# Performance work log

Measured on AMD Instinct MI355X. Metric: run time of the kernel, lower is better.

The kernel has to match this reference:

```python
import jax, jax.numpy as jnp
import numpy as np

B, T, L, E, H, V = 128, 16, 196, 512, 1024, 32000


def setup_inputs() -> dict:
    key = jax.random.key(0)
    ks = jax.random.split(key, 20)
    s = 0.02
    return {
        "caption_in": jax.random.randint(ks[0], (B, T), 0, V),
        "image_feats": jax.random.normal(ks[1], (B, L, E), jnp.float32),
        "emb": jax.random.normal(ks[2], (V, E), jnp.float32) * s,
        "W_init_h": jax.random.normal(ks[3], (E, H), jnp.float32) * s,
        "b_init_h": jnp.zeros((H,), jnp.float32),
        "W_init_c": jax.random.normal(ks[4], (E, H), jnp.float32) * s,
        "b_init_c": jnp.zeros((H,), jnp.float32),
        "W_a": jax.random.normal(ks[5], (H, H), jnp.float32) * s,
        "b_a": jnp.zeros((H,), jnp.float32),
        "U_a": jax.random.normal(ks[6], (E, H), jnp.float32) * s,
        "b_ua": jnp.zeros((H,), jnp.float32),
        "V_a": jax.random.normal(ks[7], (H, 1), jnp.float32) * s,
        "b_va": jnp.zeros((1,), jnp.float32),
        "W_beta": jax.random.normal(ks[8], (H, E), jnp.float32) * s,
        "b_beta": jnp.zeros((E,), jnp.float32),
        "W_lstm": jax.random.normal(ks[9], (2 * E, 4 * H), jnp.float32) * s,
        "U_lstm": jax.random.normal(ks[10], (H, 4 * H), jnp.float32) * s,
        "b_lstm": jnp.zeros((4 * H,), jnp.float32),
        "W_out": jax.random.normal(ks[11], (H, V), jnp.float32) * s,
        "b_out": jnp.zeros((V,), jnp.float32),
    }


def _decode(caption_in, image_feats, emb, W_init_h, b_init_h, W_init_c, b_init_c,
            W_a, b_a, U_a, b_ua, V_a, b_va, W_beta, b_beta,
            W_lstm, U_lstm, b_lstm, W_out, b_out):
    cap_emb = emb[caption_in]                      # [B,T,E]
    mean_a = jnp.mean(image_feats, axis=1)         # [B,E]
    h0 = mean_a @ W_init_h + b_init_h              # [B,H]
    c0 = mean_a @ W_init_c + b_init_c
    # attention keys: precompute U_a(h_list) once (same math as in-loop)
    keys = jnp.einsum('ble,eh->blh', image_feats, U_a) + b_ua  # [B,L,H]

    def step(carry, x_t):                          # x_t: [B,E]
        h, c = carry
        q = h @ W_a + b_a                          # [B,H]
        e = jax.nn.relu(q[:, None, :] + keys) @ V_a + b_va  # [B,L,1]
        alpha = jax.nn.softmax(e, axis=1)          # [B,L,1]
        z = jnp.sum(alpha * image_feats, axis=1)   # [B,E]
        z = z * jax.nn.sigmoid(h @ W_beta + b_beta)
        ctx = jnp.concatenate([z, x_t], axis=-1)   # [B,2E]
        gates = ctx @ W_lstm + h @ U_lstm + b_lstm # [B,4H]
        i, f, g, o = jnp.split(gates, 4, axis=-1)  # keras order i,f,c,o
        c_new = jax.nn.sigmoid(f) * c + jax.nn.sigmoid(i) * jnp.tanh(g)
        h_new = jax.nn.sigmoid(o) * jnp.tanh(c_new)
        out = jax.nn.softmax(h_new @ W_out + b_out, axis=-1)  # [B,V]
        return (h_new, c_new), out

    xs = jnp.transpose(cap_emb, (1, 0, 2))         # [T,B,E]
    _, outs = jax.lax.scan(step, (h0, c0), xs)     # [T,B,V]
    return jnp.transpose(outs, (1, 0, 2))          # [B,T,V]


def reference(caption_in, image_feats, emb, W_init_h, b_init_h, W_init_c, b_init_c,
              W_a, b_a, U_a, b_ua, V_a, b_va, W_beta, b_beta,
              W_lstm, U_lstm, b_lstm, W_out, b_out):
    return _decode(caption_in, image_feats, emb, W_init_h, b_init_h, W_init_c, b_init_c,
                   W_a, b_a, U_a, b_ua, V_a, b_va, W_beta, b_beta,
                   W_lstm, U_lstm, b_lstm, W_out, b_out)
```

## Files before the change

### kernel.cpp

```cpp
#include <hip/hip_runtime.h>
#include <hip/hip_bf16.h>
#include <math.h>

constexpr int Bc = 128, Tc = 16, Lc = 196, Ec = 512, Hc = 1024, Vc = 32000;

typedef float f32x4_t __attribute__((ext_vector_type(4)));
typedef short s16x8_t __attribute__((ext_vector_type(8)));

__device__ __forceinline__ float sigmoidf_(float x) { return 1.0f / (1.0f + expf(-x)); }

__device__ __forceinline__ unsigned short bf16rn(float x) {
    union { float f; unsigned u; } v; v.f = x;
    unsigned r = v.u + 0x7fffu + ((v.u >> 16) & 1u);
    return (unsigned short)(r >> 16);
}
__device__ __forceinline__ float bf16tof(unsigned short h) {
    union { unsigned u; float f; } v; v.u = ((unsigned)h) << 16; return v.f;
}

struct TDesc {
    const float* src;
    unsigned short* dhi;
    unsigned short* dlo;
    int N, ldd, gx, base;
};
struct PrepP {
    TDesc d[8];
    int tblocks;
    const float* feats;
    float* mean_a;
};

__global__ __launch_bounds__(256)
void prep_multi(PrepP p)
{
    const int id = blockIdx.x;
    if (id >= p.tblocks) {
        int idm = id - p.tblocks;
        int b = idm >> 1;
        int e = (idm & 1) * 256 + threadIdx.x;
        const float* f = p.feats + ((size_t)b * Lc) * Ec + e;
        float s = 0.f;
        for (int l = 0; l < Lc; ++l) s += f[(size_t)l * Ec];
        p.mean_a[b * Ec + e] = s * (1.0f / Lc);
        return;
    }
    int di = 0;
#pragma unroll
    for (int i = 1; i < 8; ++i) if (id >= p.d[i].base) di = i;
    const TDesc d = p.d[di];
    const int lid = id - d.base;
    const int k0 = (lid % d.gx) * 32;
    const int n0 = (lid / d.gx) * 32;

    __shared__ float tile[32][33];
    const int tx = threadIdx.x & 31, ty = threadIdx.x >> 5;
#pragma unroll
    for (int i = 0; i < 4; ++i)
        tile[ty + i * 8][tx] = d.src[(size_t)(k0 + ty + i * 8) * d.N + n0 + tx];
    __syncthreads();
#pragma unroll
    for (int i = 0; i < 4; ++i) {
        int nl = ty + i * 8;
        float v = tile[tx][nl];
        unsigned short hi = bf16rn(v);
        unsigned short lo = bf16rn(v - bf16tof(hi));
        size_t off = (size_t)(n0 + nl) * d.ldd + k0 + tx;
        d.dhi[off] = hi;
        d.dlo[off] = lo;
    }
}

struct GemmP {
    const float* A;
    const unsigned short* Bhi;
    const unsigned short* Blo;
    float* C;
    const float* bias;
    long ldc, cslice;
    int lda, K, gx, gy, S;
};

__device__ __forceinline__ void gemm_body(char* smem, int bx, int by, int ksl, const GemmP& p)
{
    auto As_hi = (unsigned short (*)[128][32])(smem);
    auto As_lo = (unsigned short (*)[128][32])(smem + 16384);
    auto Bs_hi = (unsigned short (*)[128][32])(smem + 32768);
    auto Bs_lo = (unsigned short (*)[128][32])(smem + 49152);

    const int t = threadIdx.x;
    const int wave = t >> 6, lane = t & 63;
    const int wr = wave >> 1, wc = wave & 1;
    const int lm = lane & 15, qd = lane >> 4;
    const size_t m0 = (size_t)bx * 128;
    const size_t n0 = (size_t)by * 128;

    const int Ksl = p.K / p.S;
    const int kbase = ksl * Ksl;

    const int srow = t >> 1;
    const int skh  = (t & 1) * 16;

    const float* Ap = p.A + (m0 + srow) * (size_t)p.lda + skh + kbase;
    const unsigned short* Bhp = p.Bhi + (n0 + srow) * (size_t)p.K + skh + kbase;
    const unsigned short* Blp = p.Blo + (n0 + srow) * (size_t)p.K + skh + kbase;

    const int nk = Ksl >> 5;
    float* Cp = p.C + (size_t)ksl * p.cslice;

    f32x4_t acc[4][4];
#pragma unroll
    for (int i = 0; i < 4; ++i)
#pragma unroll
        for (int j = 0; j < 4; ++j)
            acc[i][j] = (f32x4_t){0.f, 0.f, 0.f, 0.f};

    float av[16];
    s16x8_t sbh0, sbh1, sbl0, sbl1;

#define G_LOAD(k0_)                                              \
    do {                                                         \
        *(float4*)&av[0]  = *(const float4*)(Ap + (k0_));        \
        *(float4*)&av[4]  = *(const float4*)(Ap + (k0_) + 4);    \
        *(float4*)&av[8]  = *(const float4*)(Ap + (k0_) + 8);    \
        *(float4*)&av[12] = *(const float4*)(Ap + (k0_) + 12);   \
        sbh0 = *(const s16x8_t*)(Bhp + (k0_));                   \
        sbh1 = *(const s16x8_t*)(Bhp + (k0_) + 8);               \
        sbl0 = *(const s16x8_t*)(Blp + (k0_));                   \
        sbl1 = *(const s16x8_t*)(Blp + (k0_) + 8);               \
    } while (0)

#define LDS_STORE(buf_)                                          \
    do {                                                         \
        s16x8_t h0, h1, l0, l1;                                  \
        _Pragma("unroll")                                        \
        for (int i = 0; i < 8; ++i) {                            \
            unsigned short hi = bf16rn(av[i]);                   \
            h0[i] = (short)hi;                                   \
            l0[i] = (short)bf16rn(av[i] - bf16tof(hi));          \
        }                                                        \
        _Pragma("unroll")                                        \
        for (int i = 0; i < 8; ++i) {                            \
            unsigned short hi = bf16rn(av[8 + i]);               \
            h1[i] = (short)hi;                                   \
            l1[i] = (short)bf16rn(av[8 + i] - bf16tof(hi));      \
        }                                                        \
        *(s16x8_t*)&As_hi[buf_][srow][skh]     = h0;             \
        *(s16x8_t*)&As_hi[buf_][srow][skh + 8] = h1;             \
        *(s16x8_t*)&As_lo[buf_][srow][skh]     = l0;             \
        *(s16x8_t*)&As_lo[buf_][srow][skh + 8] = l1;             \
        *(s16x8_t*)&Bs_hi[buf_][srow][skh]     = sbh0;           \
        *(s16x8_t*)&Bs_hi[buf_][srow][skh + 8] = sbh1;           \
        *(s16x8_t*)&Bs_lo[buf_][srow][skh]     = sbl0;           \
        *(s16x8_t*)&Bs_lo[buf_][srow][skh + 8] = sbl1;           \
    } while (0)

    G_LOAD(0);
    LDS_STORE(0);
    if (nk > 1) G_LOAD(32);
    __syncthreads();

    for (int k = 0; k < nk; ++k) {
        const int cur = k & 1;
        s16x8_t ah[4], al[4], bh[4], bl[4];
#pragma unroll
        for (int mt = 0; mt < 4; ++mt) {
            ah[mt] = *(const s16x8_t*)&As_hi[cur][wr * 64 + mt * 16 + lm][qd * 8];
            al[mt] = *(const s16x8_t*)&As_lo[cur][wr * 64 + mt * 16 + lm][qd * 8];
        }
#pragma unroll
        for (int nt = 0; nt < 4; ++nt) {
            bh[nt] = *(const s16x8_t*)&Bs_hi[cur][wc * 64 + nt * 16 + lm][qd * 8];
            bl[nt] = *(const s16x8_t*)&Bs_lo[cur][wc * 64 + nt * 16 + lm][qd * 8];
        }
        if (k + 1 < nk) {
            LDS_STORE(cur ^ 1);
            if (k + 2 < nk) G_LOAD((k + 2) << 5);
        }
#pragma unroll
        for (int mt = 0; mt < 4; ++mt)
#pragma unroll
            for (int nt = 0; nt < 4; ++nt) {
                acc[mt][nt] = __builtin_amdgcn_mfma_f32_16x16x32_bf16(ah[mt], bh[nt], acc[mt][nt], 0, 0, 0);
                acc[mt][nt] = __builtin_amdgcn_mfma_f32_16x16x32_bf16(ah[mt], bl[nt], acc[mt][nt], 0, 0, 0);
                acc[mt][nt] = __builtin_amdgcn_mfma_f32_16x16x32_bf16(al[mt], bh[nt], acc[mt][nt], 0, 0, 0);
            }
        __syncthreads();
    }
#undef G_LOAD
#undef LDS_STORE

#pragma unroll
    for (int nt = 0; nt < 4; ++nt) {
        size_t n = n0 + wc * 64 + nt * 16 + lm;
        float bs = p.bias ? p.bias[n] : 0.f;
#pragma unroll
        for (int mt = 0; mt < 4; ++mt) {
#pragma unroll
            for (int r = 0; r < 4; ++r) {
                size_t m = m0 + wr * 64 + mt * 16 + qd * 4 + r;
                Cp[(size_t)m * p.ldc + n] = acc[mt][nt][r] + bs;
            }
        }
    }
}

__global__ __launch_bounds__(256)
void gemm_one(GemmP p)
{
    __shared__ __align__(16) char smem[65536];
    gemm_body(smem, blockIdx.x, blockIdx.y, blockIdx.z, p);
}

__global__ __launch_bounds__(256)
void gemm_dual(GemmP a, GemmP b)
{
    __shared__ __align__(16) char smem[65536];
    int id = blockIdx.x;
    const int na = a.gx * a.gy * a.S;
    if (id < na) {
        int by = id % a.gy; int bx = (id / a.gy) % a.gx; int kz = id / (a.gy * a.gx);
        gemm_body(smem, bx, by, kz, a);
    } else {
        id -= na;
        int by = id % b.gy; int bx = (id / b.gy) % b.gx; int kz = id / (b.gy * b.gx);
        gemm_body(smem, bx, by, kz, b);
    }
}

__global__ __launch_bounds__(256)
void concat2(const float* __restrict__ a, int na, const float* __restrict__ b, int nb,
             float* __restrict__ out)
{
    int i = blockIdx.x * 256 + threadIdx.x;
    if (i < na) out[i] = a[i];
    else if (i < na + nb) out[i] = b[i - na];
}

__global__ __launch_bounds__(256)
void mean_kernel(const float* __restrict__ feats, float* __restrict__ mean_a)
{
    int b = blockIdx.x;
    int e = blockIdx.y * 256 + threadIdx.x;
    const float* f = feats + ((size_t)b * Lc) * Ec + e;
    float s = 0.f;
    for (int l = 0; l < Lc; ++l) s += f[(size_t)l * Ec];
    mean_a[b * Ec + e] = s * (1.0f / Lc);
}

__global__ __launch_bounds__(256)
void att_scores_sk(const float* __restrict__ qp, long qstride,
                   const float* __restrict__ b_a,
                   const float* __restrict__ keys,
                   const float* __restrict__ V_a, const float* __restrict__ b_va,
                   float* __restrict__ e)
{
    int pair = blockIdx.x * 4 + (threadIdx.x >> 6);
    int lane = threadIdx.x & 63;
    int b = pair / Lc;
    const float* kp = keys + (size_t)pair * Hc;
    const float* q0 = qp + (size_t)b * 1536;
    float s = 0.f;
    for (int h = lane; h < Hc; h += 64) {
        float q = b_a[h] + q0[h] + q0[qstride + h] + q0[2 * qstride + h] + q0[3 * qstride + h];
        s = fmaf(fmaxf(q + kp[h], 0.f), V_a[h], s);
    }
#pragma unroll
    for (int off = 32; off > 0; off >>= 1) s += __shfl_down(s, off);
    if (lane == 0) e[pair] = s + b_va[0];
}

__global__ __launch_bounds__(1024)
void smv_att(float* __restrict__ out, int t,
             const float* __restrict__ qp, long qstride,
             const float* __restrict__ b_a,
             const float* __restrict__ keys,
             const float* __restrict__ V_a, const float* __restrict__ b_va,
             float* __restrict__ e)
{
    __shared__ float red[1024];
    if (blockIdx.x < 128) {
        int b = blockIdx.x;
        float* p = out + ((size_t)b * Tc + t) * (size_t)Vc;
        int tid = threadIdx.x;
        float m = -1e30f;
        for (int v = tid; v < Vc; v += 1024) m = fmaxf(m, p[v]);
        red[tid] = m; __syncthreads();
        for (int s = 512; s > 0; s >>= 1) { if (tid < s) red[tid] = fmaxf(red[tid], red[tid + s]); __syncthreads(); }
        m = red[0]; __syncthreads();
        float sum = 0.f;
        for (int v = tid; v < Vc; v += 1024) sum += expf(p[v] - m);
        red[tid] = sum; __syncthreads();
        for (int s = 512; s > 0; s >>= 1) { if (tid < s) red[tid] += red[tid + s]; __syncthreads(); }
        float inv = 1.0f / red[0];
        for (int v = tid; v < Vc; v += 1024) p[v] = expf(p[v] - m) * inv;
    } else {
        int wave = threadIdx.x >> 6, lane = threadIdx.x & 63;
        int pair = (blockIdx.x - 128) * 16 + wave;
        int b = pair / Lc;
        const float* kp = keys + (size_t)pair * Hc;
        const float* q0 = qp + (size_t)b * 1536;
        float s = 0.f;
        for (int h = lane; h < Hc; h += 64) {
            float q = b_a[h] + q0[h] + q0[qstride + h] + q0[2 * qstride + h] + q0[3 * qstride + h];
            s = fmaf(fmaxf(q + kp[h], 0.f), V_a[h], s);
        }
#pragma unroll
        for (int off = 32; off > 0; off >>= 1) s += __shfl_down(s, off);
        if (lane == 0) e[pair] = s + b_va[0];
    }
}

__global__ __launch_bounds__(256)
void zxcat_fused(const float* __restrict__ e,
                 const float* __restrict__ qp, long qstride,
                 const float* __restrict__ b_beta,
                 const int* __restrict__ caption, const float* __restrict__ emb,
                 const float* __restrict__ feats, const float* __restrict__ hc,
                 float* __restrict__ xcat, int t)
{
    int b = blockIdx.x;
    int j = blockIdx.y * 256 + threadIdx.x;
    if (blockIdx.y < 2) {
        __shared__ float red[256];
        __shared__ float alpha[Lc];
        int tid = threadIdx.x;
        float ev = (tid < Lc) ? e[b * Lc + tid] : -1e30f;
        red[tid] = ev; __syncthreads();
        for (int s = 128; s > 0; s >>= 1) { if (tid < s) red[tid] = fmaxf(red[tid], red[tid + s]); __syncthreads(); }
        float m = red[0]; __syncthreads();
        float ex = (tid < Lc) ? expf(ev - m) : 0.f;
        red[tid] = ex; __syncthreads();
        for (int s = 128; s > 0; s >>= 1) { if (tid < s) red[tid] += red[tid + s]; __syncthreads(); }
        float ssum = red[0];
        if (tid < Lc) alpha[tid] = ex / ssum;
        __syncthreads();
        const float* f = feats + ((size_t)b * Lc) * Ec + j;
        float s = 0.f;
        for (int l = 0; l < Lc; ++l) s = fmaf(alpha[l], f[(size_t)l * Ec], s);
        const float* q0 = qp + (size_t)b * 1536 + 1024 + j;
        float sb = b_beta[j] + q0[0] + q0[qstride] + q0[2 * qstride] + q0[3 * qstride];
        xcat[(size_t)b * 2048 + j] = s * sigmoidf_(sb);
    } else if (j < 2 * Ec) {
        int tok = caption[b * Tc + t];
        xcat[(size_t)b * 2048 + j] = emb[(size_t)tok * Ec + (j - Ec)];
    } else {
        xcat[(size_t)b * 2048 + j] = hc[(size_t)b * 2048 + (j - 2 * Ec)];
    }
}

__global__ __launch_bounds__(256)
void lstm_elem_sk(const float* __restrict__ gp, long gstride,
                  const float* __restrict__ b_lstm,
                  float* __restrict__ hbase, float* __restrict__ cbase, int ld)
{
    int idx = blockIdx.x * 256 + threadIdx.x;
    int b = idx >> 10;
    int j = idx & (Hc - 1);
    float gi = b_lstm[j], gf = b_lstm[Hc + j], gg = b_lstm[2 * Hc + j], go = b_lstm[3 * Hc + j];
#pragma unroll
    for (int s = 0; s < 4; ++s) {
        const float* g = gp + (size_t)s * gstride + (size_t)b * 4 * Hc;
        gi += g[j]; gf += g[Hc + j]; gg += g[2 * Hc + j]; go += g[3 * Hc + j];
    }
    float* cp = cbase + (size_t)b * ld + j;
    float* hp = hbase + (size_t)b * ld + j;
    float cn = sigmoidf_(gf) * (*cp) + sigmoidf_(gi) * tanhf(gg);
    *cp = cn;
    *hp = sigmoidf_(go) * tanhf(cn);
}

__global__ __launch_bounds__(1024)
void softmax_V(float* __restrict__ out, int t)
{
    int b = blockIdx.x;
    float* p = out + ((size_t)b * Tc + t) * (size_t)Vc;
    __shared__ float red[1024];
    int tid = threadIdx.x;
    float m = -1e30f;
    for (int v = tid; v < Vc; v += 1024) m = fmaxf(m, p[v]);
    red[tid] = m; __syncthreads();
    for (int s = 512; s > 0; s >>= 1) { if (tid < s) red[tid] = fmaxf(red[tid], red[tid + s]); __syncthreads(); }
    m = red[0]; __syncthreads();
    float sum = 0.f;
    for (int v = tid; v < Vc; v += 1024) sum += expf(p[v] - m);
    red[tid] = sum; __syncthreads();
    for (int s = 512; s > 0; s >>= 1) { if (tid < s) red[tid] += red[tid + s]; __syncthreads(); }
    float inv = 1.0f / red[0];
    for (int v = tid; v < Vc; v += 1024) p[v] = expf(p[v] - m) * inv;
}

__global__ __launch_bounds__(256)
void att_scores(const float* __restrict__ q, int ldq, const float* __restrict__ keys,
                const float* __restrict__ V_a, const float* __restrict__ b_va,
                float* __restrict__ e)
{
    int pair = blockIdx.x * 4 + (threadIdx.x >> 6);
    int lane = threadIdx.x & 63;
    int b = pair / Lc;
    const float* qp = q + (size_t)b * ldq;
    const float* kp = keys + (size_t)pair * Hc;
    float s = 0.f;
    for (int h = lane; h < Hc; h += 64)
        s = fmaf(fmaxf(qp[h] + kp[h], 0.f), V_a[h], s);
#pragma unroll
    for (int off = 32; off > 0; off >>= 1) s += __shfl_down(s, off);
    if (lane == 0) e[pair] = s + b_va[0];
}

__global__ __launch_bounds__(256)
void softmax_L(float* __restrict__ e)
{
    int b = blockIdx.x;
    float* p = e + b * Lc;
    __shared__ float red[256];
    int tid = threadIdx.x;
    float m = -1e30f;
    if (tid < Lc) m = p[tid];
    red[tid] = m; __syncthreads();
    for (int s = 128; s > 0; s >>= 1) { if (tid < s) red[tid] = fmaxf(red[tid], red[tid + s]); __syncthreads(); }
    m = red[0]; __syncthreads();
    float ex = 0.f;
    if (tid < Lc) ex = expf(p[tid] - m);
    red[tid] = ex; __syncthreads();
    for (int s = 128; s > 0; s >>= 1) { if (tid < s) red[tid] += red[tid + s]; __syncthreads(); }
    if (tid < Lc) p[tid] = ex / red[0];
}

__global__ __launch_bounds__(256)
void z_kernel(const float* __restrict__ alpha, const float* __restrict__ feats,
              float* __restrict__ z)
{
    int b = blockIdx.x;
    int e = blockIdx.y * 256 + threadIdx.x;
    const float* f = feats + ((size_t)b * Lc) * Ec + e;
    const float* a = alpha + b * Lc;
    float s = 0.f;
    for (int l = 0; l < Lc; ++l) s = fmaf(a[l], f[(size_t)l * Ec], s);
    z[b * Ec + e] = s;
}

__global__ __launch_bounds__(256)
void ctx_build(const float* __restrict__ z, const float* __restrict__ sb,
               const int* __restrict__ caption, const float* __restrict__ emb,
               float* __restrict__ ctx, int t)
{
    int b = blockIdx.x;
    int j = blockIdx.y * 256 + threadIdx.x;
    float v;
    if (j < Ec) {
        v = z[b * Ec + j] * sigmoidf_(sb[b * Ec + j]);
    } else {
        int tok = caption[b * Tc + t];
        v = emb[(size_t)tok * Ec + (j - Ec)];
    }
    ctx[b * (2 * Ec) + j] = v;
}

__global__ __launch_bounds__(256)
void lstm_elem(const float* __restrict__ gates, float* __restrict__ hbase,
               float* __restrict__ cbase, int ld)
{
    int idx = blockIdx.x * 256 + threadIdx.x;
    int b = idx >> 10;
    int j = idx & (Hc - 1);
    const float* g = gates + (size_t)b * 4 * Hc;
    float gi = g[j], gf = g[Hc + j], gg = g[2 * Hc + j], go = g[3 * Hc + j];
    float* cp = cbase + (size_t)b * ld + j;
    float* hp = hbase + (size_t)b * ld + j;
    float cn = sigmoidf_(gf) * (*cp) + sigmoidf_(gi) * tanhf(gg);
    *cp = cn;
    *hp = sigmoidf_(go) * tanhf(cn);
}

__global__ __launch_bounds__(256)
void gemm_f32(const float* __restrict__ A, int lda,
              const float* __restrict__ Bm, int ldb,
              float* __restrict__ C, int ldc,
              const float* __restrict__ bias,
              int K, int accumulate)
{
    __shared__ __align__(16) float As[16][68];
    __shared__ __align__(16) float Bs[16][68];
    const int t  = threadIdx.x;
    const int tx = t & 15;
    const int ty = t >> 4;
    const size_t m0 = (size_t)blockIdx.x * 64;
    const size_t n0 = (size_t)blockIdx.y * 64;
    const int arow = t >> 2;
    const int acol = (t & 3) << 2;
    const int brow = t >> 4;
    const int bcol = (t & 15) << 2;
    const float* Aptr = A + (m0 + arow) * (size_t)lda + acol;
    const float* Bptr = Bm + (size_t)brow * ldb + n0 + bcol;
    float acc[4][4] = {};
    for (int k0 = 0; k0 < K; k0 += 16) {
        float4 av = *reinterpret_cast<const float4*>(Aptr + k0);
        float4 bv = *reinterpret_cast<const float4*>(Bptr + (size_t)k0 * ldb);
        As[acol + 0][arow] = av.x;
        As[acol + 1][arow] = av.y;
        As[acol + 2][arow] = av.z;
        As[acol + 3][arow] = av.w;
        *reinterpret_cast<float4*>(&Bs[brow][bcol]) = bv;
        __syncthreads();
#pragma unroll
        for (int k = 0; k < 16; ++k) {
            float4 a4 = *reinterpret_cast<const float4*>(&As[k][ty << 2]);
            float4 b4 = *reinterpret_cast<const float4*>(&Bs[k][tx << 2]);
            float aa[4] = {a4.x, a4.y, a4.z, a4.w};
            float bb[4] = {b4.x, b4.y, b4.z, b4.w};
#pragma unroll
            for (int i = 0; i < 4; ++i)
#pragma unroll
                for (int j = 0; j < 4; ++j)
                    acc[i][j] = fmaf(aa[i], bb[j], acc[i][j]);
        }
        __syncthreads();
    }
    float4 bv4 = {0.f, 0.f, 0.f, 0.f};
    if (bias) bv4 = *reinterpret_cast<const float4*>(&bias[n0 + (tx << 2)]);
#pragma unroll
    for (int i = 0; i < 4; ++i) {
        size_t off = (m0 + (size_t)(ty << 2) + i) * (size_t)ldc + n0 + (tx << 2);
        float4 o;
        o.x = acc[i][0] + bv4.x;
        o.y = acc[i][1] + bv4.y;
        o.z = acc[i][2] + bv4.z;
        o.w = acc[i][3] + bv4.w;
        if (accumulate) {
            float4 prev = *reinterpret_cast<const float4*>(&C[off]);
            o.x += prev.x; o.y += prev.y; o.z += prev.z; o.w += prev.w;
        }
        *reinterpret_cast<float4*>(&C[off]) = o;
    }
}

extern "C" void kernel_launch(void* const* d_in, const int* in_sizes, int n_in,
                              void* d_out, int out_size, void* d_ws, size_t ws_size,
                              hipStream_t stream)
{
    const int*   caption  = (const int*)  d_in[0];
    const float* feats    = (const float*)d_in[1];
    const float* emb      = (const float*)d_in[2];
    const float* W_init_h = (const float*)d_in[3];
    const float* b_init_h = (const float*)d_in[4];
    const float* W_init_c = (const float*)d_in[5];
    const float* b_init_c = (const float*)d_in[6];
    const float* W_a      = (const float*)d_in[7];
    const float* b_a      = (const float*)d_in[8];
    const float* U_a      = (const float*)d_in[9];
    const float* b_ua     = (const float*)d_in[10];
    const float* V_a      = (const float*)d_in[11];
    const float* b_va     = (const float*)d_in[12];
    const float* W_beta   = (const float*)d_in[13];
    const float* b_beta   = (const float*)d_in[14];
    const float* W_lstm   = (const float*)d_in[15];
    const float* U_lstm   = (const float*)d_in[16];
    const float* b_lstm   = (const float*)d_in[17];
    const float* W_out    = (const float*)d_in[18];
    const float* b_out    = (const float*)d_in[19];
    float* out = (float*)d_out;

    dim3 blk(256);

    char* base = (char*)d_ws;
    size_t off = 0;
    auto alloc = [&](size_t bytes) { char* p = base + off; off = (off + bytes + 15) & ~(size_t)15; return p; };

    float* keys      = (float*)alloc((size_t)Bc * Lc * Hc * 4);
    float* hc        = (float*)alloc((size_t)Bc * 2048 * 4);
    float* qsb_part  = (float*)alloc((size_t)4 * Bc * 1536 * 4);
    float* e         = (float*)alloc((size_t)Bc * Lc * 4);
    float* xcat      = (float*)alloc((size_t)Bc * 2048 * 4);
    float* gate_part = (float*)alloc((size_t)4 * Bc * 4 * Hc * 4);
    float* mean_a    = (float*)alloc((size_t)Bc * Ec * 4);
    float* bcat_i    = (float*)alloc(2048 * 4);
    unsigned short* Wout_hi  = (unsigned short*)alloc((size_t)Vc * Hc * 2);
    unsigned short* Wout_lo  = (unsigned short*)alloc((size_t)Vc * Hc * 2);
    unsigned short* Wg_hi    = (unsigned short*)alloc((size_t)4096 * 2048 * 2);
    unsigned short* Wg_lo    = (unsigned short*)alloc((size_t)4096 * 2048 * 2);
    unsigned short* Wqsb_hi  = (unsigned short*)alloc((size_t)1536 * 1024 * 2);
    unsigned short* Wqsb_lo  = (unsigned short*)alloc((size_t)1536 * 1024 * 2);
    unsigned short* Ua_hi    = (unsigned short*)alloc((size_t)1024 * 512 * 2);
    unsigned short* Ua_lo    = (unsigned short*)alloc((size_t)1024 * 512 * 2);
    unsigned short* Wini_hi  = (unsigned short*)alloc((size_t)2048 * 512 * 2);
    unsigned short* Wini_lo  = (unsigned short*)alloc((size_t)2048 * 512 * 2);
    const size_t need_fast = off;

    const long QSTRIDE = (long)Bc * 1536;
    const long GSTRIDE = (long)Bc * 4 * Hc;

    if (ws_size >= need_fast) {
        PrepP pp;
        int pb = 0;
        auto addT = [&](const float* src, int N, unsigned short* dhi, unsigned short* dlo,
                        int ldd, int gx, int gy, int slot) {
            pp.d[slot] = TDesc{src, dhi, dlo, N, ldd, gx, pb};
            pb += gx * gy;
        };
        addT(W_out,    Vc,   Wout_hi, Wout_lo, 1024, 32, 1000, 0);
        addT(W_lstm,   4096, Wg_hi,   Wg_lo,   2048, 32, 128, 1);
        addT(U_lstm,   4096, Wg_hi + 1024, Wg_lo + 1024, 2048, 32, 128, 2);
        addT(W_a,      1024, Wqsb_hi, Wqsb_lo, 1024, 32, 32, 3);
        addT(W_beta,   512,  Wqsb_hi + (size_t)1024 * 1024, Wqsb_lo + (size_t)1024 * 1024, 1024, 32, 16, 4);
        addT(U_a,      1024, Ua_hi,   Ua_lo,   512, 16, 32, 5);
        addT(W_init_h, 1024, Wini_hi, Wini_lo, 512, 16, 32, 6);
        addT(W_init_c, 1024, Wini_hi + (size_t)1024 * 512, Wini_lo + (size_t)1024 * 512, 512, 16, 32, 7);
        pp.tblocks = pb;
        pp.feats = feats;
        pp.mean_a = mean_a;
        prep_multi<<<dim3(pb + 256), blk, 0, stream>>>(pp);
        concat2<<<dim3(8), blk, 0, stream>>>(b_init_h, 1024, b_init_c, 1024, bcat_i);

        auto mkg = [](const float* A, int lda, const unsigned short* bh, const unsigned short* bl,
                      float* C, long ldc, const float* bias, int K, long cslice,
                      int gx, int gy, int S) {
            GemmP p; p.A = A; p.lda = lda; p.Bhi = bh; p.Blo = bl; p.C = C; p.ldc = ldc;
            p.bias = bias; p.K = K; p.cslice = cslice; p.gx = gx; p.gy = gy; p.S = S; return p;
        };
        GemmP g_init = mkg(mean_a, Ec, Wini_hi, Wini_lo, hc, 2048, bcat_i, 512, 0, 1, 16, 1);
        GemmP g_keys = mkg(feats, Ec, Ua_hi, Ua_lo, keys, Hc, b_ua, 512, 0, 196, 8, 1);
        GemmP g_qsb  = mkg(hc, 2048, Wqsb_hi, Wqsb_lo, qsb_part, 1536, nullptr, 1024, QSTRIDE, 1, 12, 4);
        GemmP g_gate = mkg(xcat, 2048, Wg_hi, Wg_lo, gate_part, 4096, nullptr, 2048, GSTRIDE, 1, 32, 4);

        gemm_one<<<dim3(1, 16, 1), blk, 0, stream>>>(g_init);
        gemm_dual<<<dim3(196 * 8 + 48), blk, 0, stream>>>(g_keys, g_qsb);
        att_scores_sk<<<dim3((Bc * Lc) / 4), blk, 0, stream>>>(qsb_part, QSTRIDE, b_a, keys, V_a, b_va, e);

        for (int t = 0; t < Tc; ++t) {
            zxcat_fused<<<dim3(Bc, 8), blk, 0, stream>>>(e, qsb_part, QSTRIDE, b_beta, caption, emb, feats, hc, xcat, t);
            gemm_one<<<dim3(1, 32, 4), blk, 0, stream>>>(g_gate);
            lstm_elem_sk<<<dim3((Bc * Hc) / 256), blk, 0, stream>>>(gate_part, GSTRIDE, b_lstm, hc, hc + 1024, 2048);
            GemmP g_wout = mkg(hc, 2048, Wout_hi, Wout_lo, out + (size_t)t * Vc, (long)Tc * Vc, b_out, 1024, 0, 1, 250, 1);
            if (t < Tc - 1)
                gemm_dual<<<dim3(250 + 48), blk, 0, stream>>>(g_wout, g_qsb);
            else
                gemm_one<<<dim3(1, 250, 1), blk, 0, stream>>>(g_wout);
            int natt = (t < Tc - 1) ? (Bc * Lc) / 16 : 0;
            smv_att<<<dim3(128 + natt), dim3(1024), 0, stream>>>(out, t, qsb_part, QSTRIDE, b_a, keys, V_a, b_va, e);
        }
        return;
    }

    float* ws = (float*)d_ws;
    size_t foff = 0;
    float* l_keys  = ws + foff; foff += (size_t)Bc * Lc * Hc;
    float* l_h     = ws + foff; foff += (size_t)Bc * Hc;
    float* l_c     = ws + foff; foff += (size_t)Bc * Hc;
    float* l_q     = ws + foff; foff += (size_t)Bc * Hc;
    float* l_e     = ws + foff; foff += (size_t)Bc * Lc;
    float* l_sb    = ws + foff; foff += (size_t)Bc * Ec;
    float* l_z     = ws + foff; foff += (size_t)Bc * Ec;
    float* l_ctx   = ws + foff; foff += (size_t)Bc * 2 * Ec;
    float* l_gates = ws + foff; foff += (size_t)Bc * 4 * Hc;
    float* l_mean  = ws + foff; foff += (size_t)Bc * Ec;
    if (ws_size < foff * sizeof(float)) return;

    mean_kernel<<<dim3(Bc, 2), blk, 0, stream>>>(feats, l_mean);
    gemm_f32<<<dim3(Bc / 64, Hc / 64), blk, 0, stream>>>(l_mean, Ec, W_init_h, Hc, l_h, Hc, b_init_h, Ec, 0);
    gemm_f32<<<dim3(Bc / 64, Hc / 64), blk, 0, stream>>>(l_mean, Ec, W_init_c, Hc, l_c, Hc, b_init_c, Ec, 0);
    gemm_f32<<<dim3((Bc * Lc) / 64, Hc / 64), blk, 0, stream>>>(feats, Ec, U_a, Hc, l_keys, Hc, b_ua, Ec, 0);
    for (int t = 0; t < Tc; ++t) {
        gemm_f32<<<dim3(Bc / 64, Hc / 64), blk, 0, stream>>>(l_h, Hc, W_a, Hc, l_q, Hc, b_a, Hc, 0);
        att_scores<<<dim3((Bc * Lc) / 4), blk, 0, stream>>>(l_q, Hc, l_keys, V_a, b_va, l_e);
        softmax_L<<<dim3(Bc), blk, 0, stream>>>(l_e);
        z_kernel<<<dim3(Bc, 2), blk, 0, stream>>>(l_e, feats, l_z);
        gemm_f32<<<dim3(Bc / 64, Ec / 64), blk, 0, stream>>>(l_h, Hc, W_beta, Ec, l_sb, Ec, b_beta, Hc, 0);
        ctx_build<<<dim3(Bc, 4), blk, 0, stream>>>(l_z, l_sb, caption, emb, l_ctx, t);
        gemm_f32<<<dim3(Bc / 64, (4 * Hc) / 64), blk, 0, stream>>>(l_ctx, 2 * Ec, W_lstm, 4 * Hc, l_gates, 4 * Hc, b_lstm, 2 * Ec, 0);
        gemm_f32<<<dim3(Bc / 64, (4 * Hc) / 64), blk, 0, stream>>>(l_h, Hc, U_lstm, 4 * Hc, l_gates, 4 * Hc, nullptr, Hc, 1);
        lstm_elem<<<dim3((Bc * Hc) / 256), blk, 0, stream>>>(l_gates, l_h, l_c, Hc);
        gemm_f32<<<dim3(Bc / 64, Vc / 64), blk, 0, stream>>>(l_h, Hc, W_out, Vc, out + (size_t)t * Vc, Tc * Vc, b_out, Hc, 0);
        softmax_V<<<dim3(Bc), dim3(1024), 0, stream>>>(out, t);
    }
}
```

Baseline: 2.972 ms.

## Fuse attention scores, softmax and context into one per-batch kernel; precompute embeddings

Attention scoring, its softmax and the weighted context sum now run in one 1024-thread block per batch row, fused with the vocab softmax launch. This drops the separate zxcat_fused launch per step. Caption embeddings for all steps are gathered once up front into a per-step xcat buffer, and the LSTM kernel writes h directly into the next step's xcat slice. The intent is to cut one launch per step plus the global round-trip of e, at the cost of fewer, heavier attention blocks (128 instead of 1568) and a larger xcat allocation.

```diff
diff --git a/kernel.cpp b/kernel.cpp
--- a/kernel.cpp
+++ b/kernel.cpp
@@ -249,40 +249,39 @@
 }
 
 __global__ __launch_bounds__(256)
-void att_scores_sk(const float* __restrict__ qp, long qstride,
-                   const float* __restrict__ b_a,
-                   const float* __restrict__ keys,
-                   const float* __restrict__ V_a, const float* __restrict__ b_va,
-                   float* __restrict__ e)
-{
-    int pair = blockIdx.x * 4 + (threadIdx.x >> 6);
-    int lane = threadIdx.x & 63;
-    int b = pair / Lc;
-    const float* kp = keys + (size_t)pair * Hc;
-    const float* q0 = qp + (size_t)b * 1536;
-    float s = 0.f;
-    for (int h = lane; h < Hc; h += 64) {
-        float q = b_a[h] + q0[h] + q0[qstride + h] + q0[2 * qstride + h] + q0[3 * qstride + h];
-        s = fmaf(fmaxf(q + kp[h], 0.f), V_a[h], s);
-    }
-#pragma unroll
-    for (int off = 32; off > 0; off >>= 1) s += __shfl_down(s, off);
-    if (lane == 0) e[pair] = s + b_va[0];
+void xemb_h0(const int* __restrict__ caption, const float* __restrict__ emb,
+             const float* __restrict__ hc, float* __restrict__ xcat)
+{
+    const int nemb = Tc * Bc * 2;
+    int id = blockIdx.x;
+    if (id < nemb) {
+        int t = id >> 8;
+        int r = id & 255;
+        int b = r >> 1;
+        int j = (r & 1) * 256 + threadIdx.x;
+        int tok = caption[b * Tc + t];
+        xcat[(size_t)t * Bc * 2048 + (size_t)b * 2048 + 512 + j] = emb[(size_t)tok * Ec + j];
+    } else {
+        int idx = (id - nemb) * 256 + threadIdx.x;
+        int b = idx >> 10;
+        int j = idx & 1023;
+        xcat[(size_t)b * 2048 + 1024 + j] = hc[(size_t)b * 2048 + j];
+    }
 }
 
 __global__ __launch_bounds__(1024)
-void smv_att(float* __restrict__ out, int t,
-             const float* __restrict__ qp, long qstride,
-             const float* __restrict__ b_a,
-             const float* __restrict__ keys,
-             const float* __restrict__ V_a, const float* __restrict__ b_va,
-             float* __restrict__ e)
+void smv_attz(float* __restrict__ out, int t, int nsmv,
+              const float* __restrict__ qp, long qstride,
+              const float* __restrict__ b_a, const float* __restrict__ b_beta,
+              const float* __restrict__ keys,
+              const float* __restrict__ V_a, const float* __restrict__ b_va,
+              const float* __restrict__ feats, float* __restrict__ xcat_t)
 {
     __shared__ float red[1024];
-    if (blockIdx.x < 128) {
+    const int tid = threadIdx.x;
+    if (blockIdx.x < (unsigned)nsmv) {
         int b = blockIdx.x;
         float* p = out + ((size_t)b * Tc + t) * (size_t)Vc;
-        int tid = threadIdx.x;
         float m = -1e30f;
         for (int v = tid; v < Vc; v += 1024) m = fmaxf(m, p[v]);
         red[tid] = m; __syncthreads();
@@ -294,65 +293,58 @@
         for (int s = 512; s > 0; s >>= 1) { if (tid < s) red[tid] += red[tid + s]; __syncthreads(); }
         float inv = 1.0f / red[0];
         for (int v = tid; v < Vc; v += 1024) p[v] = expf(p[v] - m) * inv;
-    } else {
-        int wave = threadIdx.x >> 6, lane = threadIdx.x & 63;
-        int pair = (blockIdx.x - 128) * 16 + wave;
-        int b = pair / Lc;
-        const float* kp = keys + (size_t)pair * Hc;
-        const float* q0 = qp + (size_t)b * 1536;
-        float s = 0.f;
-        for (int h = lane; h < Hc; h += 64) {
-            float q = b_a[h] + q0[h] + q0[qstride + h] + q0[2 * qstride + h] + q0[3 * qstride + h];
-            s = fmaf(fmaxf(q + kp[h], 0.f), V_a[h], s);
-        }
-#pragma unroll
-        for (int off = 32; off > 0; off >>= 1) s += __shfl_down(s, off);
-        if (lane == 0) e[pair] = s + b_va[0];
-    }
-}
-
-__global__ __launch_bounds__(256)
-void zxcat_fused(const float* __restrict__ e,
-                 const float* __restrict__ qp, long qstride,
-                 const float* __restrict__ b_beta,
-                 const int* __restrict__ caption, const float* __restrict__ emb,
-                 const float* __restrict__ feats, const float* __restrict__ hc,
-                 float* __restrict__ xcat, int t)
-{
-    int b = blockIdx.x;
-    int j = blockIdx.y * 256 + threadIdx.x;
-    if (blockIdx.y < 2) {
-        __shared__ float red[256];
-        __shared__ float alpha[Lc];
-        int tid = threadIdx.x;
-        float ev = (tid < Lc) ? e[b * Lc + tid] : -1e30f;
-        red[tid] = ev; __syncthreads();
-        for (int s = 128; s > 0; s >>= 1) { if (tid < s) red[tid] = fmaxf(red[tid], red[tid + s]); __syncthreads(); }
-        float m = red[0]; __syncthreads();
-        float ex = (tid < Lc) ? expf(ev - m) : 0.f;
-        red[tid] = ex; __syncthreads();
-        for (int s = 128; s > 0; s >>= 1) { if (tid < s) red[tid] += red[tid + s]; __syncthreads(); }
-        float ssum = red[0];
-        if (tid < Lc) alpha[tid] = ex / ssum;
-        __syncthreads();
-        const float* f = feats + ((size_t)b * Lc) * Ec + j;
+        return;
+    }
+    __shared__ float q_lds[Hc];
+    __shared__ float va_lds[Hc];
+    __shared__ float sb_lds[Ec];
+    __shared__ float e_sm[256];
+    __shared__ float alpha[Lc];
+    const int b = blockIdx.x - nsmv;
+    const float* q0 = qp + (size_t)b * 1536;
+    q_lds[tid] = b_a[tid] + q0[tid] + q0[qstride + tid] + q0[2 * qstride + tid] + q0[3 * qstride + tid];
+    va_lds[tid] = V_a[tid];
+    if (tid < Ec) {
+        const float* qs = q0 + 1024 + tid;
+        sb_lds[tid] = b_beta[tid] + qs[0] + qs[qstride] + qs[2 * qstride] + qs[3 * qstride];
+    }
+    __syncthreads();
+    {
+        int wave = tid >> 6, lane = tid & 63;
+        float bva = b_va[0];
+        for (int l = wave; l < Lc; l += 16) {
+            const float* kp = keys + ((size_t)b * Lc + l) * Hc;
+            float s = 0.f;
+            for (int h = lane; h < Hc; h += 64)
+                s = fmaf(fmaxf(q_lds[h] + kp[h], 0.f), va_lds[h], s);
+#pragma unroll
+            for (int off = 32; off > 0; off >>= 1) s += __shfl_down(s, off);
+            if (lane == 0) e_sm[l] = s + bva;
+        }
+    }
+    __syncthreads();
+    float ev = (tid < Lc) ? e_sm[tid] : -1e30f;
+    red[tid] = ev; __syncthreads();
+    for (int s = 512; s > 0; s >>= 1) { if (tid < s) red[tid] = fmaxf(red[tid], red[tid + s]); __syncthreads(); }
+    float m = red[0]; __syncthreads();
+    float ex = (tid < Lc) ? expf(ev - m) : 0.f;
+    red[tid] = ex; __syncthreads();
+    for (int s = 512; s > 0; s >>= 1) { if (tid < s) red[tid] += red[tid + s]; __syncthreads(); }
+    if (tid < Lc) alpha[tid] = ex / red[0];
+    __syncthreads();
+    if (tid < Ec) {
+        const float* f = feats + ((size_t)b * Lc) * Ec + tid;
         float s = 0.f;
         for (int l = 0; l < Lc; ++l) s = fmaf(alpha[l], f[(size_t)l * Ec], s);
-        const float* q0 = qp + (size_t)b * 1536 + 1024 + j;
-        float sb = b_beta[j] + q0[0] + q0[qstride] + q0[2 * qstride] + q0[3 * qstride];
-        xcat[(size_t)b * 2048 + j] = s * sigmoidf_(sb);
-    } else if (j < 2 * Ec) {
-        int tok = caption[b * Tc + t];
-        xcat[(size_t)b * 2048 + j] = emb[(size_t)tok * Ec + (j - Ec)];
-    } else {
-        xcat[(size_t)b * 2048 + j] = hc[(size_t)b * 2048 + (j - 2 * Ec)];
+        xcat_t[(size_t)b * 2048 + tid] = s * sigmoidf_(sb_lds[tid]);
     }
 }
 
 __global__ __launch_bounds__(256)
 void lstm_elem_sk(const float* __restrict__ gp, long gstride,
                   const float* __restrict__ b_lstm,
-                  float* __restrict__ hbase, float* __restrict__ cbase, int ld)
+                  float* __restrict__ hbase, float* __restrict__ cbase, int ld,
+                  float* __restrict__ xh)
 {
     int idx = blockIdx.x * 256 + threadIdx.x;
     int b = idx >> 10;
@@ -364,10 +356,11 @@
         gi += g[j]; gf += g[Hc + j]; gg += g[2 * Hc + j]; go += g[3 * Hc + j];
     }
     float* cp = cbase + (size_t)b * ld + j;
-    float* hp = hbase + (size_t)b * ld + j;
     float cn = sigmoidf_(gf) * (*cp) + sigmoidf_(gi) * tanhf(gg);
     *cp = cn;
-    *hp = sigmoidf_(go) * tanhf(cn);
+    float hn = sigmoidf_(go) * tanhf(cn);
+    hbase[(size_t)b * ld + j] = hn;
+    if (xh) xh[(size_t)b * 2048 + 1024 + j] = hn;
 }
 
 __global__ __launch_bounds__(1024)
@@ -570,8 +563,7 @@
     float* keys      = (float*)alloc((size_t)Bc * Lc * Hc * 4);
     float* hc        = (float*)alloc((size_t)Bc * 2048 * 4);
     float* qsb_part  = (float*)alloc((size_t)4 * Bc * 1536 * 4);
-    float* e         = (float*)alloc((size_t)Bc * Lc * 4);
-    float* xcat      = (float*)alloc((size_t)Bc * 2048 * 4);
+    float* xcat      = (float*)alloc((size_t)Tc * Bc * 2048 * 4);
     float* gate_part = (float*)alloc((size_t)4 * Bc * 4 * Hc * 4);
     float* mean_a    = (float*)alloc((size_t)Bc * Ec * 4);
     float* bcat_i    = (float*)alloc(2048 * 4);
@@ -589,6 +581,7 @@
 
     const long QSTRIDE = (long)Bc * 1536;
     const long GSTRIDE = (long)Bc * 4 * Hc;
+    const size_t XSLICE = (size_t)Bc * 2048;
 
     if (ws_size >= need_fast) {
         PrepP pp;
@@ -621,23 +614,27 @@
         GemmP g_init = mkg(mean_a, Ec, Wini_hi, Wini_lo, hc, 2048, bcat_i, 512, 0, 1, 16, 1);
         GemmP g_keys = mkg(feats, Ec, Ua_hi, Ua_lo, keys, Hc, b_ua, 512, 0, 196, 8, 1);
         GemmP g_qsb  = mkg(hc, 2048, Wqsb_hi, Wqsb_lo, qsb_part, 1536, nullptr, 1024, QSTRIDE, 1, 12, 4);
-        GemmP g_gate = mkg(xcat, 2048, Wg_hi, Wg_lo, gate_part, 4096, nullptr, 2048, GSTRIDE, 1, 32, 4);
 
         gemm_one<<<dim3(1, 16, 1), blk, 0, stream>>>(g_init);
+        xemb_h0<<<dim3(Tc * Bc * 2 + Bc * 4), blk, 0, stream>>>(caption, emb, hc, xcat);
         gemm_dual<<<dim3(196 * 8 + 48), blk, 0, stream>>>(g_keys, g_qsb);
-        att_scores_sk<<<dim3((Bc * Lc) / 4), blk, 0, stream>>>(qsb_part, QSTRIDE, b_a, keys, V_a, b_va, e);
+        smv_attz<<<dim3(Bc), dim3(1024), 0, stream>>>(out, 0, 0, qsb_part, QSTRIDE, b_a, b_beta,
+                                                      keys, V_a, b_va, feats, xcat);
 
         for (int t = 0; t < Tc; ++t) {
-            zxcat_fused<<<dim3(Bc, 8), blk, 0, stream>>>(e, qsb_part, QSTRIDE, b_beta, caption, emb, feats, hc, xcat, t);
+            GemmP g_gate = mkg(xcat + (size_t)t * XSLICE, 2048, Wg_hi, Wg_lo, gate_part, 4096, nullptr, 2048, GSTRIDE, 1, 32, 4);
             gemm_one<<<dim3(1, 32, 4), blk, 0, stream>>>(g_gate);
-            lstm_elem_sk<<<dim3((Bc * Hc) / 256), blk, 0, stream>>>(gate_part, GSTRIDE, b_lstm, hc, hc + 1024, 2048);
+            float* xh = (t < Tc - 1) ? xcat + (size_t)(t + 1) * XSLICE : nullptr;
+            lstm_elem_sk<<<dim3((Bc * Hc) / 256), blk, 0, stream>>>(gate_part, GSTRIDE, b_lstm, hc, hc + 1024, 2048, xh);
             GemmP g_wout = mkg(hc, 2048, Wout_hi, Wout_lo, out + (size_t)t * Vc, (long)Tc * Vc, b_out, 1024, 0, 1, 250, 1);
             if (t < Tc - 1)
                 gemm_dual<<<dim3(250 + 48), blk, 0, stream>>>(g_wout, g_qsb);
             else
                 gemm_one<<<dim3(1, 250, 1), blk, 0, stream>>>(g_wout);
-            int natt = (t < Tc - 1) ? (Bc * Lc) / 16 : 0;
-            smv_att<<<dim3(128 + natt), dim3(1024), 0, stream>>>(out, t, qsb_part, QSTRIDE, b_a, keys, V_a, b_va, e);
+            int natt = (t < Tc - 1) ? Bc : 0;
+            smv_attz<<<dim3(128 + natt), dim3(1024), 0, stream>>>(out, t, 128, qsb_part, QSTRIDE, b_a, b_beta,
+                                                                  keys, V_a, b_va, feats,
+                                                                  xcat + (size_t)(t + 1) * XSLICE);
         }
         return;
     }
```

After: 3.732 ms. 25.6% more time.
